# Kernel tuning notes

Hardware: AMD Instinct MI355X
Metric: run time of the kernel (lower is better)

Reference implementation:

```python
import jax, jax.numpy as jnp
import numpy as np

NX = 768
N_HEAD = 12
N_CTX = 2048
MASKED_BIAS = -10000.0


def setup_inputs() -> dict:
    key = jax.random.key(0)
    ks = jax.random.split(key, 6)
    bs, seq = 2, N_CTX
    hidden_states = jax.random.normal(ks[0], (bs, seq, NX), dtype=jnp.float32)
    attention_mask = jnp.zeros((bs, 1, 1, seq), dtype=jnp.float32)
    # Conv1D params: out = x @ W + b, W: (in, out)
    w_attn = jax.random.normal(ks[1], (NX, 3 * NX), dtype=jnp.float32) * 0.02
    b_attn = jnp.zeros((3 * NX,), dtype=jnp.float32)
    w_proj = jax.random.normal(ks[2], (NX, NX), dtype=jnp.float32) * 0.02
    b_proj = jnp.zeros((NX,), dtype=jnp.float32)
    return {
        "hidden_states": hidden_states,
        "attention_mask": attention_mask,
        "w_attn": w_attn,
        "b_attn": b_attn,
        "w_proj": w_proj,
        "b_proj": b_proj,
    }


def reference(hidden_states, attention_mask, w_attn, b_attn, w_proj, b_proj):
    bs, seq, _ = hidden_states.shape
    hd = NX // N_HEAD  # 64
    qkv = hidden_states @ w_attn + b_attn  # [bs, seq, 3*nx]
    query, key, value = jnp.split(qkv, 3, axis=2)
    # Faithful to source: direct reshape (NOT standard split-heads transpose)
    q = query.reshape(bs, N_HEAD, seq, hd)
    k = key.reshape(bs, N_HEAD, seq, hd)
    v = value.reshape(bs, N_HEAD, seq, hd)
    w = jnp.einsum("bhqd,bhkd->bhqk", q, k) / jnp.sqrt(jnp.float32(hd))
    # causal mask: tril, sliced as bias[:, :, ns-nd:ns, :ns] with nd=ns=seq
    mask = jnp.tril(jnp.ones((seq, seq), dtype=jnp.float32))[None, None]
    w = w * mask + MASKED_BIAS * (1.0 - mask)
    w = w + attention_mask
    w = jax.nn.softmax(w, axis=-1)  # dropout = identity (eval mode)
    a = jnp.einsum("bhqk,bhkd->bhqd", w, v)
    a = a.transpose(0, 2, 1, 3).reshape(bs, seq, NX)
    a = a @ w_proj + b_proj  # resid dropout = identity
    return a
```

## Files before the change

### kernel.cpp

```cpp
#include <hip/hip_runtime.h>
#include <hip/hip_bf16.h>

typedef unsigned short u16;
typedef short bf16x8 __attribute__((ext_vector_type(8)));
typedef float f32x4 __attribute__((ext_vector_type(4)));

#define NXC 768
#define NHEAD 12
#define SEQ 2048
#define BSZ 2
#define HD 64
#define NCHUNK 40
#define LOG2E 1.4426950408889634f

__device__ inline u16 f2bf(float f) {
    unsigned int u = __float_as_uint(f);
    unsigned int r = u + 0x7fffu + ((u >> 16) & 1u);
    return (u16)(r >> 16);
}
__device__ inline unsigned pk2(float lo, float hi) {
    return (unsigned)f2bf(lo) | ((unsigned)f2bf(hi) << 16);
}
__device__ inline uint4 ldcvt(const float* p) {
    float4 a = *(const float4*)p;
    float4 b = *(const float4*)(p + 4);
    uint4 o;
    o.x = pk2(a.x, a.y); o.y = pk2(a.z, a.w);
    o.z = pk2(b.x, b.y); o.w = pk2(b.z, b.w);
    return o;
}
__device__ inline float ex2(float x) { return __builtin_amdgcn_exp2f(x); }

__global__ void transpose_cast_kernel(const float* __restrict__ in, u16* __restrict__ out,
                                      int R, int C) {
    __shared__ float tile[32][33];
    int cb = blockIdx.x * 32, rb = blockIdx.y * 32;
    int tx = threadIdx.x, ty = threadIdx.y;
    #pragma unroll
    for (int i = 0; i < 32; i += 8)
        tile[ty + i][tx] = in[(size_t)(rb + ty + i) * C + cb + tx];
    __syncthreads();
    #pragma unroll
    for (int i = 0; i < 32; i += 8)
        out[(size_t)(cb + ty + i) * R + rb + tx] = f2bf(tile[tx][ty + i]);
}

__global__ __launch_bounds__(256) void vt_kernel(const u16* __restrict__ Vb,
                                                 u16* __restrict__ Vtg) {
    __shared__ u16 tile[64][68];
    int y = blockIdx.y;
    size_t base = (size_t)y * (SEQ * HD);
    int ss0 = blockIdx.x * 64;
    int t = threadIdx.x;
    #pragma unroll
    for (int c = t; c < 512; c += 256) {
        int r = c >> 3, col = (c & 7) * 8;
        *(uint4*)&tile[r][col] = *(const uint4*)&Vb[base + (size_t)(ss0 + r) * HD + col];
    }
    __syncthreads();
    #pragma unroll
    for (int c = t; c < 512; c += 256) {
        int dd = c >> 3, s8 = (c & 7) * 8;
        ushort4 a, bq;
        a.x = tile[s8 + 0][dd]; a.y = tile[s8 + 1][dd];
        a.z = tile[s8 + 2][dd]; a.w = tile[s8 + 3][dd];
        bq.x = tile[s8 + 4][dd]; bq.y = tile[s8 + 5][dd];
        bq.z = tile[s8 + 6][dd]; bq.w = tile[s8 + 7][dd];
        u16* dst = &Vtg[base + (size_t)dd * SEQ + ss0 + s8];
        *(ushort4*)dst = a;
        *(ushort4*)(dst + 4) = bq;
    }
}

template <int EPI>
__global__ __launch_bounds__(256) void gemm_bt_kernel(
    const void* __restrict__ Av, const u16* __restrict__ BT,
    const float* __restrict__ bias,
    u16* __restrict__ outQ, u16* __restrict__ outK, u16* __restrict__ outV,
    float* __restrict__ outF,
    int M, int N, int K) {
    __shared__ u16 As[128 * 32];
    __shared__ u16 Bs[64 * 32];
    int tileM = blockIdx.y * 128, tileN = blockIdx.x * 64;
    int t = threadIdx.x;
    int lane = t & 63, wave = t >> 6;
    int wm = wave * 32;
    int quad = lane >> 4, l16 = lane & 15;
    f32x4 acc[2][4] = {};

    int r0 = t >> 2, c0 = (t & 3) * 8;
    const float* Af0 = (const float*)Av + (size_t)(tileM + r0) * K + c0;
    const float* Af1 = Af0 + (size_t)64 * K;
    const u16*   Ab0 = (const u16*)Av + (size_t)(tileM + r0) * K + c0;
    const u16*   Ab1 = Ab0 + (size_t)64 * K;
    const u16* Bg0 = BT + (size_t)(tileN + r0) * K + c0;
    u16* AsW0 = &As[r0 * 32 + c0];
    u16* AsW1 = &As[(r0 + 64) * 32 + c0];
    u16* BsW0 = &Bs[(r0 & 63) * 32 + c0];

    uint4 ra0, ra1, rb0;
    if (EPI == 0) { ra0 = ldcvt(Af0); ra1 = ldcvt(Af1); }
    else          { ra0 = *(const uint4*)(Ab0); ra1 = *(const uint4*)(Ab1); }
    rb0 = *(const uint4*)(Bg0);

    for (int k0 = 0; k0 < K; k0 += 32) {
        __syncthreads();
        *(uint4*)AsW0 = ra0;
        *(uint4*)AsW1 = ra1;
        *(uint4*)BsW0 = rb0;
        __syncthreads();
        if (k0 + 32 < K) {
            if (EPI == 0) { ra0 = ldcvt(Af0 + k0 + 32); ra1 = ldcvt(Af1 + k0 + 32); }
            else          { ra0 = *(const uint4*)(Ab0 + k0 + 32); ra1 = *(const uint4*)(Ab1 + k0 + 32); }
            rb0 = *(const uint4*)(Bg0 + k0 + 32);
        }
        bf16x8 af[2], bfr[4];
        #pragma unroll
        for (int i = 0; i < 2; ++i)
            af[i] = *(const bf16x8*)&As[(wm + i * 16 + l16) * 32 + quad * 8];
        #pragma unroll
        for (int j = 0; j < 4; ++j)
            bfr[j] = *(const bf16x8*)&Bs[(j * 16 + l16) * 32 + quad * 8];
        #pragma unroll
        for (int i = 0; i < 2; ++i)
            #pragma unroll
            for (int j = 0; j < 4; ++j)
                acc[i][j] = __builtin_amdgcn_mfma_f32_16x16x32_bf16(af[i], bfr[j], acc[i][j], 0, 0, 0);
    }

    #pragma unroll
    for (int i = 0; i < 2; ++i) {
        #pragma unroll
        for (int j = 0; j < 4; ++j) {
            int n = tileN + j * 16 + l16;
            float bv = bias[n];
            #pragma unroll
            for (int r = 0; r < 4; ++r) {
                int m = tileM + wm + i * 16 + quad * 4 + r;
                float v = acc[i][j][r] + bv;
                if (EPI == 0) {
                    if (n < 768) {
                        outQ[(size_t)m * 768 + n] = f2bf(v);
                    } else if (n < 1536) {
                        outK[(size_t)m * 768 + (n - 768)] = f2bf(v * (0.125f * LOG2E));
                    } else {
                        outV[(size_t)m * 768 + (n - 1536)] = f2bf(v);
                    }
                } else {
                    outF[(size_t)m * N + n] = v;
                }
            }
        }
    }
}

__global__ __launch_bounds__(256) void attn_mfma_kernel(
    const u16* __restrict__ Q, const u16* __restrict__ Kg,
    const u16* __restrict__ Vtg, const float* __restrict__ amask,
    u16* __restrict__ Opart, float* __restrict__ Lpart) {
    __shared__ u16 Ks[64][72];
    __shared__ u16 Vt[64][72];
    __shared__ u16 Ps[4][2][16][72];
    __shared__ float Ams[64];

    int bh = blockIdx.y;
    int b = bh / NHEAD, h = bh % NHEAD;
    int p = NCHUNK - 1 - (int)blockIdx.x;
    int bx = 15, c = 0, a = 0;
    #pragma unroll
    for (int i = 0; i < 16; ++i) {
        int n = (i >> 2) + 1;
        if (p < a + n) { bx = i; c = p - a; break; }
        a += n;
    }
    int kbase = c * 512;
    int nt = 2 * (bx + 1) - 8 * c;
    if (nt > 8) nt = 8;

    int t = threadIdx.x;
    int w = t >> 6, lane = t & 63;
    int quad = lane >> 4, l16 = lane & 15;
    size_t headbase = (size_t)b * (SEQ * NXC) + (size_t)h * (SEQ * HD);
    size_t headbaseT = (size_t)(b * NHEAD + h) * (SEQ * HD);

    int r0 = bx * 128;
    int qw0 = r0 + w * 32;
    bf16x8 qf[2][2];
    #pragma unroll
    for (int g = 0; g < 2; ++g)
        #pragma unroll
        for (int s = 0; s < 2; ++s)
            qf[g][s] = *(const bf16x8*)&Q[headbase + (size_t)(qw0 + g * 16 + l16) * HD + s * 32 + quad * 8];

    float l_part[2] = {0.f, 0.f};
    f32x4 o[2][4] = {};

    int pr_row = t >> 3, pr_col = (t & 7) * 8;
    uint4 kr0, kr1, vr0, vr1; float amr;
    {
        int k0 = kbase;
        kr0 = *(const uint4*)&Kg[headbase + (size_t)(k0 + pr_row) * HD + pr_col];
        kr1 = *(const uint4*)&Kg[headbase + (size_t)(k0 + pr_row + 32) * HD + pr_col];
        vr0 = *(const uint4*)&Vtg[headbaseT + (size_t)pr_row * SEQ + k0 + pr_col];
        vr1 = *(const uint4*)&Vtg[headbaseT + (size_t)(pr_row + 32) * SEQ + k0 + pr_col];
        if (t < 64) amr = amask[(size_t)b * SEQ + k0 + t];
    }

    for (int kt = 0; kt < nt; ++kt) {
        int k0 = kbase + kt * 64;
        __syncthreads();
        *(uint4*)&Ks[pr_row][pr_col] = kr0;
        *(uint4*)&Ks[pr_row + 32][pr_col] = kr1;
        *(uint4*)&Vt[pr_row][pr_col] = vr0;
        *(uint4*)&Vt[pr_row + 32][pr_col] = vr1;
        if (t < 64) Ams[t] = amr * LOG2E;
        __syncthreads();
        if (kt + 1 < nt) {
            int kn = k0 + 64;
            kr0 = *(const uint4*)&Kg[headbase + (size_t)(kn + pr_row) * HD + pr_col];
            kr1 = *(const uint4*)&Kg[headbase + (size_t)(kn + pr_row + 32) * HD + pr_col];
            vr0 = *(const uint4*)&Vtg[headbaseT + (size_t)pr_row * SEQ + kn + pr_col];
            vr1 = *(const uint4*)&Vtg[headbaseT + (size_t)(pr_row + 32) * SEQ + kn + pr_col];
            if (t < 64) amr = amask[(size_t)b * SEQ + kn + t];
        }

        if (k0 > qw0 + 31) continue;
        bool act0 = (k0 <= qw0 + 15);

        bf16x8 kf[2][4];
        #pragma unroll
        for (int s = 0; s < 2; ++s)
            #pragma unroll
            for (int j = 0; j < 4; ++j)
                kf[s][j] = *(const bf16x8*)&Ks[j * 16 + l16][s * 32 + quad * 8];
        float4 am4[4];
        #pragma unroll
        for (int j = 0; j < 4; ++j)
            am4[j] = *(const float4*)&Ams[j * 16 + quad * 4];

        #pragma unroll
        for (int g = 0; g < 2; ++g) {
            if (g == 0 && !act0) continue;
            int qg0 = qw0 + g * 16;
            int qrow = qg0 + l16;
            f32x4 sacc[4] = {};
            #pragma unroll
            for (int s = 0; s < 2; ++s)
                #pragma unroll
                for (int j = 0; j < 4; ++j)
                    sacc[j] = __builtin_amdgcn_mfma_f32_16x16x32_bf16(kf[s][j], qf[g][s], sacc[j], 0, 0, 0);

            bool diag = (k0 + 63 > qg0);
            #pragma unroll
            for (int j = 0; j < 4; ++j) {
                float pv[4];
                float am[4] = {am4[j].x, am4[j].y, am4[j].z, am4[j].w};
                #pragma unroll
                for (int r = 0; r < 4; ++r) {
                    float pp = ex2(sacc[j][r] + am[r]);
                    if (diag && (k0 + j * 16 + quad * 4 + r > qrow)) pp = 0.f;
                    pv[r] = pp;
                }
                l_part[g] += (pv[0] + pv[1]) + (pv[2] + pv[3]);
                unsigned pk01 = ((__float_as_uint(pv[0]) + 0x8000u) >> 16) |
                                ((__float_as_uint(pv[1]) + 0x8000u) & 0xffff0000u);
                unsigned pk23 = ((__float_as_uint(pv[2]) + 0x8000u) >> 16) |
                                ((__float_as_uint(pv[3]) + 0x8000u) & 0xffff0000u);
                *(uint2*)&Ps[w][g][l16][j * 16 + quad * 4] = make_uint2(pk01, pk23);
            }
        }

        #pragma unroll
        for (int s = 0; s < 2; ++s) {
            bf16x8 pf1 = *(const bf16x8*)&Ps[w][1][l16][s * 32 + quad * 8];
            bf16x8 pf0;
            if (act0) pf0 = *(const bf16x8*)&Ps[w][0][l16][s * 32 + quad * 8];
            #pragma unroll
            for (int dc = 0; dc < 4; ++dc) {
                bf16x8 vf = *(const bf16x8*)&Vt[dc * 16 + l16][s * 32 + quad * 8];
                if (act0) o[0][dc] = __builtin_amdgcn_mfma_f32_16x16x32_bf16(pf0, vf, o[0][dc], 0, 0, 0);
                o[1][dc] = __builtin_amdgcn_mfma_f32_16x16x32_bf16(pf1, vf, o[1][dc], 0, 0, 0);
            }
        }
    }

    u16* Ob = Opart + ((size_t)bh * NCHUNK + p) * (128 * 64);
    float* Lb = Lpart + ((size_t)bh * NCHUNK + p) * 128;
    #pragma unroll
    for (int g = 0; g < 2; ++g) {
        float l = l_part[g] + __shfl_xor(l_part[g], 16);
        l += __shfl_xor(l, 32);
        #pragma unroll
        for (int dc = 0; dc < 4; ++dc)
            #pragma unroll
            for (int r = 0; r < 4; ++r) {
                int rl = w * 32 + g * 16 + quad * 4 + r;
                Ob[rl * 64 + dc * 16 + l16] = f2bf(o[g][dc][r]);
            }
        if (quad == 0) Lb[w * 32 + g * 16 + l16] = l;
    }
}

__global__ __launch_bounds__(256) void attn_combine_kernel(
    const u16* __restrict__ Opart, const float* __restrict__ Lpart,
    u16* __restrict__ Aout) {
    __shared__ float winv[32];
    int bh = blockIdx.y;
    int b = bh / NHEAD, h = bh % NHEAD;
    int row0 = blockIdx.x * 32;
    int bx = row0 >> 7;
    int g = bx >> 2;
    int nch = g + 1;
    int p0 = 2 * g * (g + 1) + (bx & 3) * (g + 1);
    int rbase = row0 & 127;
    int t = threadIdx.x;

    if (t < 32) {
        float L = 0.f;
        for (int c = 0; c < nch; ++c)
            L += Lpart[((size_t)bh * NCHUNK + p0 + c) * 128 + rbase + t];
        winv[t] = 1.0f / L;
    }
    __syncthreads();

    int row = t >> 3;
    int d0 = (t & 7) * 8;
    int rl = rbase + row;
    float acc[8] = {};
    for (int c = 0; c < nch; ++c) {
        uint4 u = *(const uint4*)&Opart[(((size_t)bh * NCHUNK + p0 + c) * 128 + rl) * 64 + d0];
        acc[0] += __uint_as_float(u.x << 16);
        acc[1] += __uint_as_float(u.x & 0xffff0000u);
        acc[2] += __uint_as_float(u.y << 16);
        acc[3] += __uint_as_float(u.y & 0xffff0000u);
        acc[4] += __uint_as_float(u.z << 16);
        acc[5] += __uint_as_float(u.z & 0xffff0000u);
        acc[6] += __uint_as_float(u.w << 16);
        acc[7] += __uint_as_float(u.w & 0xffff0000u);
    }
    float s = winv[row];
    uint4 o;
    o.x = pk2(acc[0] * s, acc[1] * s);
    o.y = pk2(acc[2] * s, acc[3] * s);
    o.z = pk2(acc[4] * s, acc[5] * s);
    o.w = pk2(acc[6] * s, acc[7] * s);
    *(uint4*)&Aout[((size_t)b * SEQ + row0 + row) * NXC + h * HD + d0] = o;
}

extern "C" void kernel_launch(void* const* d_in, const int* in_sizes, int n_in,
                              void* d_out, int out_size, void* d_ws, size_t ws_size,
                              hipStream_t stream) {
    const float* hs     = (const float*)d_in[0];
    const float* amask  = (const float*)d_in[1];
    const float* w_attn = (const float*)d_in[2];
    const float* b_attn = (const float*)d_in[3];
    const float* w_proj = (const float*)d_in[4];
    const float* b_proj = (const float*)d_in[5];
    float* out = (float*)d_out;

    const int M = BSZ * SEQ;
    char* ws = (char*)d_ws;
    auto alloc = [&](size_t bytes) {
        char* p = ws;
        ws += (bytes + 255) & ~(size_t)255;
        return p;
    };
    u16* WaT    = (u16*)alloc((size_t)3 * NXC * NXC * 2);
    u16* WpT    = (u16*)alloc((size_t)NXC * NXC * 2);
    u16* Qb     = (u16*)alloc((size_t)M * NXC * 2);
    u16* Kb     = (u16*)alloc((size_t)M * NXC * 2);
    u16* Vb     = (u16*)alloc((size_t)M * NXC * 2);
    u16* Vtg    = (u16*)alloc((size_t)M * NXC * 2);
    u16* Ab     = (u16*)alloc((size_t)M * NXC * 2);
    u16* Opart  = (u16*)alloc((size_t)BSZ * NHEAD * NCHUNK * 128 * 64 * 2);
    float* Lpart = (float*)alloc((size_t)BSZ * NHEAD * NCHUNK * 128 * 4);

    transpose_cast_kernel<<<dim3(3 * NXC / 32, NXC / 32), dim3(32, 8), 0, stream>>>(w_attn, WaT, NXC, 3 * NXC);
    transpose_cast_kernel<<<dim3(NXC / 32, NXC / 32), dim3(32, 8), 0, stream>>>(w_proj, WpT, NXC, NXC);

    gemm_bt_kernel<0><<<dim3(3 * NXC / 64, M / 128), dim3(256), 0, stream>>>(
        hs, WaT, b_attn, Qb, Kb, Vb, nullptr, M, 3 * NXC, NXC);
    vt_kernel<<<dim3(SEQ / 64, BSZ * NHEAD), dim3(256), 0, stream>>>(Vb, Vtg);
    attn_mfma_kernel<<<dim3(NCHUNK, BSZ * NHEAD), dim3(256), 0, stream>>>(
        Qb, Kb, Vtg, amask, Opart, Lpart);
    attn_combine_kernel<<<dim3(SEQ / 32, BSZ * NHEAD), dim3(256), 0, stream>>>(
        Opart, Lpart, Ab);
    gemm_bt_kernel<1><<<dim3(NXC / 64, M / 128), dim3(256), 0, stream>>>(
        Ab, WpT, b_proj, nullptr, nullptr, nullptr, out, M, NXC, NXC);
}
```

Measured before the change: 179.9 us.

## Pre-cast hidden states to bf16 and deepen GEMM K-tile to 64 with padded LDS

Adds a separate cast kernel that converts hidden_states to bf16 once, so the QKV GEMM no longer converts fp32 to bf16 inside its load loop. The GEMM now loads a 64-wide K slice per iteration into LDS rows padded to 72 elements, halving the barrier count and aiming to reduce bank conflicts. In exchange it adds an extra kernel launch plus a full read and write of the activations, and uses more LDS per block.

After: 284.2 us. 58.0% more time.

```diff
diff --git a/kernel.cpp b/kernel.cpp
--- a/kernel.cpp
+++ b/kernel.cpp
@@ -21,15 +21,16 @@
 __device__ inline unsigned pk2(float lo, float hi) {
     return (unsigned)f2bf(lo) | ((unsigned)f2bf(hi) << 16);
 }
-__device__ inline uint4 ldcvt(const float* p) {
-    float4 a = *(const float4*)p;
-    float4 b = *(const float4*)(p + 4);
-    uint4 o;
-    o.x = pk2(a.x, a.y); o.y = pk2(a.z, a.w);
-    o.z = pk2(b.x, b.y); o.w = pk2(b.z, b.w);
-    return o;
-}
 __device__ inline float ex2(float x) { return __builtin_amdgcn_exp2f(x); }
+
+__global__ void cast4_kernel(const float* __restrict__ in, u16* __restrict__ out, int n4) {
+    int i = blockIdx.x * 256 + threadIdx.x;
+    if (i >= n4) return;
+    float4 v = ((const float4*)in)[i];
+    ushort4 o;
+    o.x = f2bf(v.x); o.y = f2bf(v.y); o.z = f2bf(v.z); o.w = f2bf(v.w);
+    ((ushort4*)out)[i] = o;
+}
 
 __global__ void transpose_cast_kernel(const float* __restrict__ in, u16* __restrict__ out,
                                       int R, int C) {
@@ -74,13 +75,13 @@
 
 template <int EPI>
 __global__ __launch_bounds__(256) void gemm_bt_kernel(
-    const void* __restrict__ Av, const u16* __restrict__ BT,
+    const u16* __restrict__ A, const u16* __restrict__ BT,
     const float* __restrict__ bias,
     u16* __restrict__ outQ, u16* __restrict__ outK, u16* __restrict__ outV,
     float* __restrict__ outF,
     int M, int N, int K) {
-    __shared__ u16 As[128 * 32];
-    __shared__ u16 Bs[64 * 32];
+    __shared__ u16 As[128 * 72];
+    __shared__ u16 Bs[64 * 72];
     int tileM = blockIdx.y * 128, tileN = blockIdx.x * 64;
     int t = threadIdx.x;
     int lane = t & 63, wave = t >> 6;
@@ -88,44 +89,46 @@
     int quad = lane >> 4, l16 = lane & 15;
     f32x4 acc[2][4] = {};
 
-    int r0 = t >> 2, c0 = (t & 3) * 8;
-    const float* Af0 = (const float*)Av + (size_t)(tileM + r0) * K + c0;
-    const float* Af1 = Af0 + (size_t)64 * K;
-    const u16*   Ab0 = (const u16*)Av + (size_t)(tileM + r0) * K + c0;
-    const u16*   Ab1 = Ab0 + (size_t)64 * K;
-    const u16* Bg0 = BT + (size_t)(tileN + r0) * K + c0;
-    u16* AsW0 = &As[r0 * 32 + c0];
-    u16* AsW1 = &As[(r0 + 64) * 32 + c0];
-    u16* BsW0 = &Bs[(r0 & 63) * 32 + c0];
-
-    uint4 ra0, ra1, rb0;
-    if (EPI == 0) { ra0 = ldcvt(Af0); ra1 = ldcvt(Af1); }
-    else          { ra0 = *(const uint4*)(Ab0); ra1 = *(const uint4*)(Ab1); }
-    rb0 = *(const uint4*)(Bg0);
-
-    for (int k0 = 0; k0 < K; k0 += 32) {
+    int rr = t >> 3, cc = (t & 7) * 8;
+    const u16* Ag = A + (size_t)(tileM + rr) * K + cc;
+    const u16* Bg = BT + (size_t)(tileN + rr) * K + cc;
+    u16* AsW = &As[rr * 72 + cc];
+    u16* BsW = &Bs[rr * 72 + cc];
+
+    uint4 ra[4], rb[2];
+    #pragma unroll
+    for (int i = 0; i < 4; ++i) ra[i] = *(const uint4*)(Ag + (size_t)32 * i * K);
+    #pragma unroll
+    for (int i = 0; i < 2; ++i) rb[i] = *(const uint4*)(Bg + (size_t)32 * i * K);
+
+    for (int k0 = 0; k0 < K; k0 += 64) {
         __syncthreads();
-        *(uint4*)AsW0 = ra0;
-        *(uint4*)AsW1 = ra1;
-        *(uint4*)BsW0 = rb0;
+        #pragma unroll
+        for (int i = 0; i < 4; ++i) *(uint4*)(AsW + i * 32 * 72) = ra[i];
+        #pragma unroll
+        for (int i = 0; i < 2; ++i) *(uint4*)(BsW + i * 32 * 72) = rb[i];
         __syncthreads();
-        if (k0 + 32 < K) {
-            if (EPI == 0) { ra0 = ldcvt(Af0 + k0 + 32); ra1 = ldcvt(Af1 + k0 + 32); }
-            else          { ra0 = *(const uint4*)(Ab0 + k0 + 32); ra1 = *(const uint4*)(Ab1 + k0 + 32); }
-            rb0 = *(const uint4*)(Bg0 + k0 + 32);
-        }
-        bf16x8 af[2], bfr[4];
-        #pragma unroll
-        for (int i = 0; i < 2; ++i)
-            af[i] = *(const bf16x8*)&As[(wm + i * 16 + l16) * 32 + quad * 8];
-        #pragma unroll
-        for (int j = 0; j < 4; ++j)
-            bfr[j] = *(const bf16x8*)&Bs[(j * 16 + l16) * 32 + quad * 8];
-        #pragma unroll
-        for (int i = 0; i < 2; ++i)
+        if (k0 + 64 < K) {
+            #pragma unroll
+            for (int i = 0; i < 4; ++i) ra[i] = *(const uint4*)(Ag + (size_t)32 * i * K + k0 + 64);
+            #pragma unroll
+            for (int i = 0; i < 2; ++i) rb[i] = *(const uint4*)(Bg + (size_t)32 * i * K + k0 + 64);
+        }
+        #pragma unroll
+        for (int s = 0; s < 2; ++s) {
+            bf16x8 af[2], bfr[4];
+            #pragma unroll
+            for (int i = 0; i < 2; ++i)
+                af[i] = *(const bf16x8*)&As[(wm + i * 16 + l16) * 72 + s * 32 + quad * 8];
             #pragma unroll
             for (int j = 0; j < 4; ++j)
-                acc[i][j] = __builtin_amdgcn_mfma_f32_16x16x32_bf16(af[i], bfr[j], acc[i][j], 0, 0, 0);
+                bfr[j] = *(const bf16x8*)&Bs[(j * 16 + l16) * 72 + s * 32 + quad * 8];
+            #pragma unroll
+            for (int i = 0; i < 2; ++i)
+                #pragma unroll
+                for (int j = 0; j < 4; ++j)
+                    acc[i][j] = __builtin_amdgcn_mfma_f32_16x16x32_bf16(af[i], bfr[j], acc[i][j], 0, 0, 0);
+        }
     }
 
     #pragma unroll
@@ -365,6 +368,7 @@
         ws += (bytes + 255) & ~(size_t)255;
         return p;
     };
+    u16* HSbf   = (u16*)alloc((size_t)M * NXC * 2);
     u16* WaT    = (u16*)alloc((size_t)3 * NXC * NXC * 2);
     u16* WpT    = (u16*)alloc((size_t)NXC * NXC * 2);
     u16* Qb     = (u16*)alloc((size_t)M * NXC * 2);
@@ -375,11 +379,14 @@
     u16* Opart  = (u16*)alloc((size_t)BSZ * NHEAD * NCHUNK * 128 * 64 * 2);
     float* Lpart = (float*)alloc((size_t)BSZ * NHEAD * NCHUNK * 128 * 4);
 
-    transpose_cast_kernel<<<dim3(3 * NXC / 32, NXC / 32), dim3(32, 8), 0, stream>>>(w_attn, WaT, NXC, 3 * NXC);
-    transpose_cast_kernel<<<dim3(NXC / 32, NXC / 32), dim3(32, 8), 0, stream>>>(w_proj, WpT, NXC, NXC);
-
+    {
+        int n4 = M * NXC / 4;
+        cast4_kernel<<<dim3((n4 + 255) / 256), dim3(256), 0, stream>>>(hs, HSbf, n4);
+        transpose_cast_kernel<<<dim3(3 * NXC / 32, NXC / 32), dim3(32, 8), 0, stream>>>(w_attn, WaT, NXC, 3 * NXC);
+        transpose_cast_kernel<<<dim3(NXC / 32, NXC / 32), dim3(32, 8), 0, stream>>>(w_proj, WpT, NXC, NXC);
+    }
     gemm_bt_kernel<0><<<dim3(3 * NXC / 64, M / 128), dim3(256), 0, stream>>>(
-        hs, WaT, b_attn, Qb, Kb, Vb, nullptr, M, 3 * NXC, NXC);
+        HSbf, WaT, b_attn, Qb, Kb, Vb, nullptr, M, 3 * NXC, NXC);
     vt_kernel<<<dim3(SEQ / 64, BSZ * NHEAD), dim3(256), 0, stream>>>(Vb, Vtg);
     attn_mfma_kernel<<<dim3(NCHUNK, BSZ * NHEAD), dim3(256), 0, stream>>>(
         Qb, Kb, Vtg, amask, Opart, Lpart);
```
